# Kernel optimization log

Hardware: AMD Instinct MI355X
Metric: run time of the kernel (lower is better)

The kernel has to match this reference:

```python
import jax, jax.numpy as jnp
import numpy as np

X_SIZE, NUM_NEURONS, Z_SIZE = 2048, 4096, 64
D = X_SIZE + NUM_NEURONS + Z_SIZE  # 6208
TOPK, ZTOPK = 16, 8
EPS_TIE = 1e-9
RND = 0.5  # stand-in for random.random(); tie indicator t is 0 w.p. 1 for continuous inputs


def setup_inputs() -> dict:
    key = jax.random.key(0)
    k1, k2, k3, k4, k5 = jax.random.split(key, 5)
    x = jax.random.normal(k1, (X_SIZE,), dtype=jnp.float32)
    z = jax.random.normal(k2, (Z_SIZE,), dtype=jnp.float32)
    y_response = jax.random.uniform(k3, (NUM_NEURONS,), dtype=jnp.float32)
    neurons = jax.random.normal(k4, (D, D), dtype=jnp.float32)
    ages = 1.0 + 9.0 * jax.random.uniform(k5, (D,), dtype=jnp.float32)  # ages >= 1
    return {"x": x, "z": z, "y_response": y_response, "neurons": neurons, "ages": ages}


def _update_rows(neurons, ages, inpt, idx, vals):
    # Faithful to update_neuron_weights, including the (1,k)@(k,D) row-mix
    # that broadcasts the same mixed row to all k winner rows.
    a = ages[idx]                                   # (k,)
    upd = (vals / a)[:, None] * inpt[None, :]       # (k, D)
    mix = jnp.einsum('k,kd->d', (a - 1.0) / a, neurons[idx])  # (D,)
    new_rows = mix[None, :] + upd                   # (k, D)
    norm = jnp.sqrt(jnp.sum(new_rows * new_rows, axis=1, keepdims=True)) + 1e-12
    neurons = neurons.at[idx].set(new_rows / norm)
    ages = ages.at[idx].add(1.0)
    return neurons, ages


def reference(x, z, y_response, neurons, ages):
    # Steady-state path: num_neurons_init == max_num_neurons (> topk),
    # supervized_z = supervized_x = None, xtopk = None.
    x0, x1 = 0, X_SIZE
    y0, y1 = X_SIZE, X_SIZE + NUM_NEURONS
    z0 = X_SIZE + NUM_NEURONS

    inpt = jnp.concatenate([x, y_response, z])      # (D,)
    response = neurons @ inpt                       # (D,)
    final = jnp.zeros_like(response)

    # --- z path: top-(ztopk) winners, normalized against runner-up ---
    zvals, zidx = jax.lax.top_k(response[z0:], ZTOPK + 1)
    gz = z0 + zidx
    final = final.at[gz[:-1]].set((zvals[:-1] - zvals[-1]) / (zvals[0] - zvals[-1]))
    neurons, ages = _update_rows(neurons, ages, inpt, gz[:-1], zvals[:-1])

    # --- x path (xtopk None, unsupervised): normalize full x response ---
    rx = response[x0:x1]
    tx = jnp.where(jnp.all(rx == 0.0), 1.0, 0.0)
    xvals = rx / (jnp.max(rx) + EPS_TIE * tx * RND)
    final = final.at[x0:x1].set(xvals)
    xidx = jnp.arange(x0, x1)
    neurons, ages = _update_rows(neurons, ages, inpt, xidx[:-1], xvals[:-1])

    # --- y path: fully grown net -> topk winner-take-most branch ---
    yvals, yidx = jax.lax.top_k(response[y0:y1], TOPK + 1)
    gy = y0 + yidx
    ty = jnp.where(jnp.any(yvals[:-1] == yvals[-1]), 1.0, 0.0)
    final = final.at[gy[:-1]].set(
        (yvals[:-1] - yvals[-1]) / (yvals[0] - yvals[-1] + EPS_TIE * ty * RND))
    neurons, ages = _update_rows(neurons, ages, inpt, gy[:-1], yvals[:-1])

    z_response = final[z0:]
    return z_response, final, neurons, ages
```

## Files before the change

kernel.cpp:

```cpp
#include <hip/hip_runtime.h>
#include <math.h>

typedef float v4f __attribute__((ext_vector_type(4)));

#define XS 2048
#define NN 4096
#define ZS 64
#define DD 6208
#define D4 1552
#define Z0 (XS + NN)
#define TOPK 16
#define ZTOPK 8
#define EPS_TIE 1e-9f
#define RNDC 0.5f
#define NXUPD 2047

#define OUT_FINAL 64
#define OUT_NEUR  (64 + DD)
#define OUT_AGES  (OUT_NEUR + (size_t)DD * DD)

#define WS_RESP   0
#define WS_INPT   DD
#define WS_MIXX   (2 * DD)
#define WS_MIXZ   (3 * DD)
#define WS_MIXY   (4 * DD)
#define WS_SCAL   (5 * DD)
#define WS_SELROW (WS_SCAL + 32)
#define WS_SELC   (WS_SELROW + 24)
#define WS_SELW   (WS_SELC + 24)
#define WS_TOTAL  (WS_SELW + 32)

#define XBLKS 1024
#define CSPL  388

__device__ __forceinline__ v4f ld4(const float* p) { return *(const v4f*)p; }
__device__ __forceinline__ v4f v4z() { v4f v; v.x = v.y = v.z = v.w = 0.f; return v; }
__device__ __forceinline__ float dot4(v4f a, v4f b) {
  return fmaf(a.x, b.x, fmaf(a.y, b.y, fmaf(a.z, b.z, a.w * b.w)));
}
__device__ __forceinline__ v4f load_inpt(const float* x, const float* yr,
                                         const float* zv, int c) {
  int col = c * 4;
  if (col < XS) return ld4(x + col);
  if (col < Z0) return ld4(yr + (col - XS));
  return ld4(zv + (col - Z0));
}

__global__ __launch_bounds__(256) void k_phase1(
    const float* __restrict__ x, const float* __restrict__ yr,
    const float* __restrict__ zv, const float* __restrict__ neurons,
    const float* __restrict__ ages, float* __restrict__ ws,
    float* __restrict__ outn)
{
  const int t = threadIdx.x;
  const int b = blockIdx.x;

  if (b < XBLKS) {
    const int rg = b >> 2, cs = b & 3;
    const int row0 = rg * 8;
    const int cbase = cs * CSPL;
    const int c0 = cbase + t;
    const int c1 = cbase + 256 + t;
    const bool has1 = (t < CSPL - 256);

    v4f i0 = load_inpt(x, yr, zv, c0);
    v4f i1 = has1 ? load_inpt(x, yr, zv, c1) : v4z();
    if (b < 4) {
      ((v4f*)(ws + WS_INPT))[c0] = i0;
      if (has1) ((v4f*)(ws + WS_INPT))[c1] = i1;
    }

    float wr[8];
    #pragma unroll
    for (int r = 0; r < 8; ++r) {
      float a = ages[row0 + r];
      wr[r] = (row0 + r < NXUPD) ? (a - 1.f) / a : 0.f;
    }

    float dot[8];
    v4f m0 = v4z(), m1 = v4z();
    #pragma unroll
    for (int r = 0; r < 8; ++r) {
      const int row = row0 + r;
      const float* rp = neurons + (size_t)row * DD;
      v4f a0 = ld4(rp + 4 * c0);
      v4f a1 = has1 ? ld4(rp + 4 * c1) : v4z();
      dot[r] = dot4(a0, i0) + dot4(a1, i1);
      m0 += wr[r] * a0;
      m1 += wr[r] * a1;
      if (row >= NXUPD) {
        __builtin_nontemporal_store(a0, (v4f*)(outn + (size_t)row * DD + 4 * c0));
        if (has1)
          __builtin_nontemporal_store(a1, (v4f*)(outn + (size_t)row * DD + 4 * c1));
      }
    }

    __shared__ float wred[4][8];
    const int lane = t & 63, wv = t >> 6;
    #pragma unroll
    for (int r = 0; r < 8; ++r) {
      float v = dot[r];
      #pragma unroll
      for (int m = 32; m >= 1; m >>= 1) v += __shfl_xor(v, m);
      if (lane == 0) wred[wv][r] = v;
    }
    __syncthreads();
    if (t < 8)
      atomicAdd(ws + WS_RESP + row0 + t,
                wred[0][t] + wred[1][t] + wred[2][t] + wred[3][t]);

    atomicAdd(ws + WS_MIXX + 4 * c0 + 0, m0.x);
    atomicAdd(ws + WS_MIXX + 4 * c0 + 1, m0.y);
    atomicAdd(ws + WS_MIXX + 4 * c0 + 2, m0.z);
    atomicAdd(ws + WS_MIXX + 4 * c0 + 3, m0.w);
    if (has1) {
      atomicAdd(ws + WS_MIXX + 4 * c1 + 0, m1.x);
      atomicAdd(ws + WS_MIXX + 4 * c1 + 1, m1.y);
      atomicAdd(ws + WS_MIXX + 4 * c1 + 2, m1.z);
      atomicAdd(ws + WS_MIXX + 4 * c1 + 3, m1.w);
    }
  } else {
    const int row = 2048 + (b - XBLKS);
    const float* rp = neurons + (size_t)row * DD;
    float* op = outn + (size_t)row * DD;
    float dot = 0.f;
    #pragma unroll
    for (int k = 0; k < 6; ++k) {
      const int c = t + 256 * k;
      v4f a = ld4(rp + 4 * c);
      v4f iv = load_inpt(x, yr, zv, c);
      dot += dot4(a, iv);
      __builtin_nontemporal_store(a, (v4f*)(op + 4 * c));
    }
    if (t < 16) {
      const int c = 1536 + t;
      v4f a = ld4(rp + 4 * c);
      v4f iv = ld4(zv + (4 * c - Z0));
      dot += dot4(a, iv);
      __builtin_nontemporal_store(a, (v4f*)(op + 4 * c));
    }
    __shared__ float red[4];
    const int lane = t & 63, wv = t >> 6;
    #pragma unroll
    for (int m = 32; m >= 1; m >>= 1) dot += __shfl_xor(dot, m);
    if (lane == 0) red[wv] = dot;
    __syncthreads();
    if (t == 0) ws[WS_RESP + row] = red[0] + red[1] + red[2] + red[3];
  }
}

__global__ __launch_bounds__(1024) void k_phase2(
    const float* __restrict__ ages, float* __restrict__ ws, float* __restrict__ out)
{
  const int t = threadIdx.x;
  __shared__ float sv[NN];
  __shared__ float swv[64];
  __shared__ int   swi[16];
  __shared__ float s_zval[ZTOPK + 1];
  __shared__ int   s_zidx[ZTOPK + 1];
  __shared__ float s_yval[TOPK + 1];
  __shared__ int   s_yidx[TOPK + 1];
  __shared__ float s_denx, s_ty;
  __shared__ float s_z64[ZS];

  float* resp = ws + WS_RESP;

  if (t < ZS) s_z64[t] = resp[Z0 + t];
  __syncthreads();
  if (t < 64) {
    float v = s_z64[t];
    for (int j = 0; j <= ZTOPK; ++j) {
      float bv = v; int bi = t;
      #pragma unroll
      for (int m = 1; m < 64; m <<= 1) {
        float ov = __shfl_xor(bv, m);
        int   oi = __shfl_xor(bi, m);
        if (ov > bv || (ov == bv && oi < bi)) { bv = ov; bi = oi; }
      }
      if (t == 0) { s_zval[j] = bv; s_zidx[j] = bi; }
      if (t == bi) v = -INFINITY;
    }
  }

  float lm = -INFINITY; int nz = 0;
  for (int i = t; i < XS; i += 1024) { float v = resp[i]; lm = fmaxf(lm, v); nz |= (v != 0.f); }
  #pragma unroll
  for (int m = 1; m < 64; m <<= 1) { lm = fmaxf(lm, __shfl_xor(lm, m)); nz |= __shfl_xor(nz, m); }
  if ((t & 63) == 0) { swv[t >> 6] = lm; swi[t >> 6] = nz; }
  __syncthreads();
  if (t == 0) {
    float m2 = -INFINITY; int n2 = 0;
    for (int q = 0; q < 16; ++q) { m2 = fmaxf(m2, swv[q]); n2 |= swi[q]; }
    float tx = n2 ? 0.f : 1.f;
    s_denx = m2 + EPS_TIE * tx * RNDC;
  }
  __syncthreads();

  for (int i = t; i < NN; i += 1024) sv[i] = resp[XS + i];
  __syncthreads();
  for (int j = 0; j <= TOPK; ++j) {
    float bv = -INFINITY; int bi = 0x7fffffff;
    for (int i = t; i < NN; i += 1024) { float v = sv[i]; if (v > bv || (v == bv && i < bi)) { bv = v; bi = i; } }
    #pragma unroll
    for (int m = 1; m < 64; m <<= 1) {
      float ov = __shfl_xor(bv, m); int oi = __shfl_xor(bi, m);
      if (ov > bv || (ov == bv && oi < bi)) { bv = ov; bi = oi; }
    }
    if ((t & 63) == 0) { swv[t >> 6] = bv; swi[t >> 6] = bi; }
    __syncthreads();
    if (t == 0) {
      float b2 = -INFINITY; int i2 = 0x7fffffff;
      for (int q = 0; q < 16; ++q)
        if (swv[q] > b2 || (swv[q] == b2 && swi[q] < i2)) { b2 = swv[q]; i2 = swi[q]; }
      s_yval[j] = b2; s_yidx[j] = i2; sv[i2] = -INFINITY;
    }
    __syncthreads();
  }
  if (t == 0) {
    float ty = 0.f;
    for (int q = 0; q < TOPK; ++q) if (s_yval[q] == s_yval[TOPK]) ty = 1.f;
    s_ty = ty;
  }
  __syncthreads();

  const float denx  = s_denx;
  const float zlast = s_zval[ZTOPK];
  const float zden  = s_zval[0] - zlast;
  const float ylast = s_yval[TOPK];
  const float yden  = s_yval[0] - ylast + EPS_TIE * s_ty * RNDC;
  float* fin = out + OUT_FINAL;
  for (int i = t; i < DD; i += 1024) {
    float v = 0.f;
    if (i < XS) v = resp[i] / denx;
    fin[i] = v;
  }
  __syncthreads();
  if (t < ZTOPK)                  fin[Z0 + s_zidx[t]] = (s_zval[t] - zlast) / zden;
  else if (t >= 32 && t < 32 + TOPK) { int k = t - 32; fin[XS + s_yidx[k]] = (s_yval[k] - ylast) / yden; }
  if (t >= 128 && t < 192) {
    int i = t - 128;
    float v = 0.f;
    for (int k = 0; k < ZTOPK; ++k) if (s_zidx[k] == i) v = (s_zval[k] - zlast) / zden;
    out[i] = v;
  }

  float* oag = out + OUT_AGES;
  for (int i = t; i < DD; i += 1024) oag[i] = ages[i] + ((i < NXUPD) ? 1.f : 0.f);
  __syncthreads();
  if (t < ZTOPK + TOPK) {
    int row = (t < ZTOPK) ? (Z0 + s_zidx[t]) : (XS + s_yidx[t - ZTOPK]);
    oag[row] = ages[row] + 1.f;
  }

  float sii = 0.f, smm = 0.f, smi = 0.f;
  float* inpt = ws + WS_INPT;
  float* mixx = ws + WS_MIXX;
  for (int i = t; i < DD; i += 1024) {
    float ip = inpt[i], mx = mixx[i];
    sii = fmaf(ip, ip, sii); smm = fmaf(mx, mx, smm); smi = fmaf(mx, ip, smi);
  }
  #pragma unroll
  for (int m = 1; m < 64; m <<= 1) {
    sii += __shfl_xor(sii, m); smm += __shfl_xor(smm, m); smi += __shfl_xor(smi, m);
  }
  __syncthreads();
  if ((t & 63) == 0) { int w = t >> 6; swv[w] = sii; swv[16 + w] = smm; swv[32 + w] = smi; }
  __syncthreads();
  if (t == 0) {
    float a = 0.f, b = 0.f, c = 0.f;
    for (int q = 0; q < 16; ++q) { a += swv[q]; b += swv[16 + q]; c += swv[32 + q]; }
    float* scal = ws + WS_SCAL;
    scal[0] = a; scal[1] = b; scal[2] = c; scal[7] = denx;
  }

  if (t < ZTOPK) {
    int row = Z0 + s_zidx[t];
    ((int*)(ws + WS_SELROW))[t] = row;
    float a = ages[row];
    ws[WS_SELC + t] = s_zval[t] / a;
    ws[WS_SELW + t] = (a - 1.f) / a;
  } else if (t >= 32 && t < 32 + TOPK) {
    int k = t - 32;
    int row = XS + s_yidx[k];
    ((int*)(ws + WS_SELROW))[ZTOPK + k] = row;
    float a = ages[row];
    ws[WS_SELC + ZTOPK + k] = s_yval[k] / a;
    ws[WS_SELW + ZTOPK + k] = (a - 1.f) / a;
  }
}

__global__ __launch_bounds__(256) void k_phase3a(
    const float* __restrict__ neurons, float* __restrict__ ws)
{
  const int b = blockIdx.x;
  const int t = threadIdx.x;
  const int row = ((const int*)(ws + WS_SELROW))[b];
  const float w = ws[WS_SELW + b];
  float* dst = ws + ((b < ZTOPK) ? WS_MIXZ : WS_MIXY);
  const float* src = neurons + (size_t)row * DD;
  #pragma unroll
  for (int k = 0; k < 6; ++k) {
    const int c = t + 256 * k;
    v4f a = ld4(src + 4 * c);
    atomicAdd(dst + 4 * c + 0, w * a.x);
    atomicAdd(dst + 4 * c + 1, w * a.y);
    atomicAdd(dst + 4 * c + 2, w * a.z);
    atomicAdd(dst + 4 * c + 3, w * a.w);
  }
  if (t < 16) {
    const int c = 1536 + t;
    v4f a = ld4(src + 4 * c);
    atomicAdd(dst + 4 * c + 0, w * a.x);
    atomicAdd(dst + 4 * c + 1, w * a.y);
    atomicAdd(dst + 4 * c + 2, w * a.z);
    atomicAdd(dst + 4 * c + 3, w * a.w);
  }
}

__global__ __launch_bounds__(1024) void k_phase3b(float* __restrict__ ws)
{
  const int t = threadIdx.x;
  __shared__ float red[64];
  float* inpt = ws + WS_INPT;
  float smmz = 0.f, smiz = 0.f, smmy = 0.f, smiy = 0.f;
  for (int i = t; i < DD; i += 1024) {
    float ip = inpt[i];
    float mz = ws[WS_MIXZ + i], my = ws[WS_MIXY + i];
    smmz = fmaf(mz, mz, smmz); smiz = fmaf(mz, ip, smiz);
    smmy = fmaf(my, my, smmy); smiy = fmaf(my, ip, smiy);
  }
  #pragma unroll
  for (int m = 1; m < 64; m <<= 1) {
    smmz += __shfl_xor(smmz, m); smiz += __shfl_xor(smiz, m);
    smmy += __shfl_xor(smmy, m); smiy += __shfl_xor(smiy, m);
  }
  __syncthreads();
  if ((t & 63) == 0) { int w = t >> 6; red[w] = smmz; red[16 + w] = smiz; red[32 + w] = smmy; red[48 + w] = smiy; }
  __syncthreads();
  if (t == 0) {
    float a = 0.f, b = 0.f, c = 0.f, d = 0.f;
    for (int q = 0; q < 16; ++q) { a += red[q]; b += red[16 + q]; c += red[32 + q]; d += red[48 + q]; }
    ws[WS_SCAL + 3] = a; ws[WS_SCAL + 4] = b; ws[WS_SCAL + 5] = c; ws[WS_SCAL + 6] = d;
  }
}

__global__ __launch_bounds__(256) void k_phase4(
    const float* __restrict__ ages, const float* __restrict__ ws,
    float* __restrict__ outn)
{
  const int b = blockIdx.x;
  const int t = threadIdx.x;
  const float sii = ws[WS_SCAL + 0];
  int row; float c, smm, smi; const float* mix;
  if (b < NXUPD) {
    row = b;
    float a = ages[row];
    c = (ws[WS_RESP + row] / ws[WS_SCAL + 7]) / a;
    mix = ws + WS_MIXX; smm = ws[WS_SCAL + 1]; smi = ws[WS_SCAL + 2];
  } else {
    int k = b - NXUPD;
    row = ((const int*)(ws + WS_SELROW))[k];
    c = ws[WS_SELC + k];
    if (k < ZTOPK) { mix = ws + WS_MIXZ; smm = ws[WS_SCAL + 3]; smi = ws[WS_SCAL + 4]; }
    else           { mix = ws + WS_MIXY; smm = ws[WS_SCAL + 5]; smi = ws[WS_SCAL + 6]; }
  }
  const float inv = 1.f / (sqrtf(fmaf(c, fmaf(c, sii, 2.f * smi), smm)) + 1e-12f);
  const float* inpt = ws + WS_INPT;
  float* dst = outn + (size_t)row * DD;
  #pragma unroll
  for (int k = 0; k < 6; ++k) {
    const int i = t + 256 * k;
    v4f m4 = ((const v4f*)(mix))[i];
    v4f i4 = ((const v4f*)(inpt))[i];
    v4f o = (m4 + c * i4) * inv;
    __builtin_nontemporal_store(o, (v4f*)dst + i);
  }
  if (t < 16) {
    const int i = 1536 + t;
    v4f m4 = ((const v4f*)(mix))[i];
    v4f i4 = ((const v4f*)(inpt))[i];
    v4f o = (m4 + c * i4) * inv;
    __builtin_nontemporal_store(o, (v4f*)dst + i);
  }
}

extern "C" void kernel_launch(void* const* d_in, const int* in_sizes, int n_in,
                              void* d_out, int out_size, void* d_ws, size_t ws_size,
                              hipStream_t stream)
{
  (void)in_sizes; (void)n_in; (void)out_size; (void)ws_size;
  const float* x    = (const float*)d_in[0];
  const float* zin  = (const float*)d_in[1];
  const float* yr   = (const float*)d_in[2];
  const float* neur = (const float*)d_in[3];
  const float* ages = (const float*)d_in[4];
  float* out = (float*)d_out;
  float* ws  = (float*)d_ws;

  hipMemsetAsync(d_ws, 0, (size_t)WS_TOTAL * sizeof(float), stream);
  k_phase1<<<XBLKS + (DD - XS), 256, 0, stream>>>(x, yr, zin, neur, ages, ws, out + OUT_NEUR);
  k_phase2<<<1, 1024, 0, stream>>>(ages, ws, out);
  k_phase3a<<<ZTOPK + TOPK, 256, 0, stream>>>(neur, ws);
  k_phase3b<<<1, 1024, 0, stream>>>(ws);
  k_phase4<<<NXUPD + ZTOPK + TOPK, 256, 0, stream>>>(ages, ws, out + OUT_NEUR);
}
```

Before: 359.2 us.

## Replace MIXX atomics with staged partials, parallelize top-k, offload ages/final init

Phase1 x-blocks now write their per-row-group mix partials into the output neuron buffer as scratch rows instead of issuing float atomics to a shared workspace vector. Extra blocks in phase3a then reduce those 256 partial rows column-wise. Phase2's single-block top-k is restructured into per-wave local top-k followed by a one-wave merge, which removes many block-wide barriers. Ages and zero-fill of final are moved into auxiliary phase1 blocks, and all norm reductions are merged into phase3b. The scratch use of the output buffer relies on phase4 later overwriting those rows, and it adds a strided column read over 256 rows.

```diff
diff --git a/kernel.cpp b/kernel.cpp
--- a/kernel.cpp
+++ b/kernel.cpp
@@ -32,6 +32,10 @@
 
 #define XBLKS 1024
 #define CSPL  388
+#define YZBLKS (DD - XS)
+#define AUXBLKS 11
+
+#define RBLKS 388
 
 __device__ __forceinline__ v4f ld4(const float* p) { return *(const v4f*)p; }
 __device__ __forceinline__ v4f v4z() { v4f v; v.x = v.y = v.z = v.w = 0.f; return v; }
@@ -45,15 +49,24 @@
   if (col < Z0) return ld4(yr + (col - XS));
   return ld4(zv + (col - Z0));
 }
+__device__ __forceinline__ v4f wred4(v4f a) {
+  #pragma unroll
+  for (int m = 32; m >= 1; m >>= 1) {
+    a.x += __shfl_xor(a.x, m); a.y += __shfl_xor(a.y, m);
+    a.z += __shfl_xor(a.z, m); a.w += __shfl_xor(a.w, m);
+  }
+  return a;
+}
 
 __global__ __launch_bounds__(256) void k_phase1(
     const float* __restrict__ x, const float* __restrict__ yr,
     const float* __restrict__ zv, const float* __restrict__ neurons,
     const float* __restrict__ ages, float* __restrict__ ws,
-    float* __restrict__ outn)
+    float* __restrict__ out)
 {
   const int t = threadIdx.x;
   const int b = blockIdx.x;
+  float* outn = out + OUT_NEUR;
 
   if (b < XBLKS) {
     const int rg = b >> 2, cs = b & 3;
@@ -109,17 +122,10 @@
       atomicAdd(ws + WS_RESP + row0 + t,
                 wred[0][t] + wred[1][t] + wred[2][t] + wred[3][t]);
 
-    atomicAdd(ws + WS_MIXX + 4 * c0 + 0, m0.x);
-    atomicAdd(ws + WS_MIXX + 4 * c0 + 1, m0.y);
-    atomicAdd(ws + WS_MIXX + 4 * c0 + 2, m0.z);
-    atomicAdd(ws + WS_MIXX + 4 * c0 + 3, m0.w);
-    if (has1) {
-      atomicAdd(ws + WS_MIXX + 4 * c1 + 0, m1.x);
-      atomicAdd(ws + WS_MIXX + 4 * c1 + 1, m1.y);
-      atomicAdd(ws + WS_MIXX + 4 * c1 + 2, m1.z);
-      atomicAdd(ws + WS_MIXX + 4 * c1 + 3, m1.w);
-    }
-  } else {
+    float* pm = outn + (size_t)rg * DD;
+    *(v4f*)(pm + 4 * c0) = m0;
+    if (has1) *(v4f*)(pm + 4 * c1) = m1;
+  } else if (b < XBLKS + YZBLKS) {
     const int row = 2048 + (b - XBLKS);
     const float* rp = neurons + (size_t)row * DD;
     float* op = outn + (size_t)row * DD;
@@ -146,6 +152,19 @@
     if (lane == 0) red[wv] = dot;
     __syncthreads();
     if (t == 0) ws[WS_RESP + row] = red[0] + red[1] + red[2] + red[3];
+  } else {
+    const int e = b - (XBLKS + YZBLKS);
+    const int base = e * 1024;
+    #pragma unroll
+    for (int k = 0; k < 4; ++k) {
+      int j = base + t + 256 * k;
+      if (j < DD) {
+        out[OUT_AGES + j] = ages[j] + ((j < NXUPD) ? 1.f : 0.f);
+      } else {
+        int f = j - DD;
+        if (f < DD - XS) out[OUT_FINAL + XS + f] = 0.f;
+      }
+    }
   }
 }
 
@@ -153,194 +172,217 @@
     const float* __restrict__ ages, float* __restrict__ ws, float* __restrict__ out)
 {
   const int t = threadIdx.x;
-  __shared__ float sv[NN];
-  __shared__ float swv[64];
-  __shared__ int   swi[16];
+  const int lane = t & 63, wv = t >> 6;
+  __shared__ float s_candv[16 * (TOPK + 1)];
+  __shared__ int   s_candi[16 * (TOPK + 1)];
   __shared__ float s_zval[ZTOPK + 1];
   __shared__ int   s_zidx[ZTOPK + 1];
   __shared__ float s_yval[TOPK + 1];
   __shared__ int   s_yidx[TOPK + 1];
+  __shared__ float s_red[16];
+  __shared__ int   s_redi[16];
   __shared__ float s_denx, s_ty;
-  __shared__ float s_z64[ZS];
 
   float* resp = ws + WS_RESP;
-
-  if (t < ZS) s_z64[t] = resp[Z0 + t];
-  __syncthreads();
-  if (t < 64) {
-    float v = s_z64[t];
-    for (int j = 0; j <= ZTOPK; ++j) {
-      float bv = v; int bi = t;
+  float* fin  = out + OUT_FINAL;
+  float* oag  = out + OUT_AGES;
+
+  {
+    float v0 = resp[t], v1 = resp[t + 1024];
+    float lm = fmaxf(v0, v1);
+    int nz = (v0 != 0.f) | (v1 != 0.f);
+    #pragma unroll
+    for (int m = 1; m < 64; m <<= 1) { lm = fmaxf(lm, __shfl_xor(lm, m)); nz |= __shfl_xor(nz, m); }
+    if (lane == 0) { s_red[wv] = lm; s_redi[wv] = nz; }
+  }
+
+  {
+    float v[4]; int id[4];
+    #pragma unroll
+    for (int q = 0; q < 4; ++q) { int i = (wv << 8) + (q << 6) + lane; id[q] = i; v[q] = resp[XS + i]; }
+    for (int j = 0; j <= TOPK; ++j) {
+      float bv = v[0]; int bi = id[0];
+      #pragma unroll
+      for (int q = 1; q < 4; ++q)
+        if (v[q] > bv || (v[q] == bv && id[q] < bi)) { bv = v[q]; bi = id[q]; }
       #pragma unroll
       for (int m = 1; m < 64; m <<= 1) {
-        float ov = __shfl_xor(bv, m);
-        int   oi = __shfl_xor(bi, m);
+        float ov = __shfl_xor(bv, m); int oi = __shfl_xor(bi, m);
         if (ov > bv || (ov == bv && oi < bi)) { bv = ov; bi = oi; }
       }
-      if (t == 0) { s_zval[j] = bv; s_zidx[j] = bi; }
-      if (t == bi) v = -INFINITY;
-    }
-  }
-
-  float lm = -INFINITY; int nz = 0;
-  for (int i = t; i < XS; i += 1024) { float v = resp[i]; lm = fmaxf(lm, v); nz |= (v != 0.f); }
-  #pragma unroll
-  for (int m = 1; m < 64; m <<= 1) { lm = fmaxf(lm, __shfl_xor(lm, m)); nz |= __shfl_xor(nz, m); }
-  if ((t & 63) == 0) { swv[t >> 6] = lm; swi[t >> 6] = nz; }
+      if (lane == 0) { s_candv[wv * (TOPK + 1) + j] = bv; s_candi[wv * (TOPK + 1) + j] = bi; }
+      #pragma unroll
+      for (int q = 0; q < 4; ++q) if (id[q] == bi) v[q] = -INFINITY;
+    }
+  }
+
+  if (wv == 0) {
+    float v = resp[Z0 + lane];
+    for (int j = 0; j <= ZTOPK; ++j) {
+      float bv = v; int bi = lane;
+      #pragma unroll
+      for (int m = 1; m < 64; m <<= 1) {
+        float ov = __shfl_xor(bv, m); int oi = __shfl_xor(bi, m);
+        if (ov > bv || (ov == bv && oi < bi)) { bv = ov; bi = oi; }
+      }
+      if (lane == 0) { s_zval[j] = bv; s_zidx[j] = bi; }
+      if (lane == bi) v = -INFINITY;
+    }
+  }
+
   __syncthreads();
-  if (t == 0) {
+
+  if (t == 64) {
     float m2 = -INFINITY; int n2 = 0;
-    for (int q = 0; q < 16; ++q) { m2 = fmaxf(m2, swv[q]); n2 |= swi[q]; }
-    float tx = n2 ? 0.f : 1.f;
-    s_denx = m2 + EPS_TIE * tx * RNDC;
+    for (int q = 0; q < 16; ++q) { m2 = fmaxf(m2, s_red[q]); n2 |= s_redi[q]; }
+    float dx = m2 + EPS_TIE * (n2 ? 0.f : 1.f) * RNDC;
+    s_denx = dx;
+    ws[WS_SCAL + 7] = dx;
+  }
+  if (wv == 0) {
+    float mv[5]; int mi[5];
+    #pragma unroll
+    for (int q = 0; q < 5; ++q) {
+      int k = lane + (q << 6);
+      if (k < 16 * (TOPK + 1)) { mv[q] = s_candv[k]; mi[q] = s_candi[k]; }
+      else { mv[q] = -INFINITY; mi[q] = 0x7fffffff; }
+    }
+    for (int j = 0; j <= TOPK; ++j) {
+      float bv = mv[0]; int bi = mi[0];
+      #pragma unroll
+      for (int q = 1; q < 5; ++q)
+        if (mv[q] > bv || (mv[q] == bv && mi[q] < bi)) { bv = mv[q]; bi = mi[q]; }
+      #pragma unroll
+      for (int m = 1; m < 64; m <<= 1) {
+        float ov = __shfl_xor(bv, m); int oi = __shfl_xor(bi, m);
+        if (ov > bv || (ov == bv && oi < bi)) { bv = ov; bi = oi; }
+      }
+      if (lane == 0) { s_yval[j] = bv; s_yidx[j] = bi; }
+      #pragma unroll
+      for (int q = 0; q < 5; ++q) if (mi[q] == bi) mv[q] = -INFINITY;
+    }
+    if (lane == 0) {
+      float ty = 0.f;
+      for (int q = 0; q < TOPK; ++q) if (s_yval[q] == s_yval[TOPK]) ty = 1.f;
+      s_ty = ty;
+    }
   }
   __syncthreads();
 
-  for (int i = t; i < NN; i += 1024) sv[i] = resp[XS + i];
-  __syncthreads();
-  for (int j = 0; j <= TOPK; ++j) {
-    float bv = -INFINITY; int bi = 0x7fffffff;
-    for (int i = t; i < NN; i += 1024) { float v = sv[i]; if (v > bv || (v == bv && i < bi)) { bv = v; bi = i; } }
-    #pragma unroll
-    for (int m = 1; m < 64; m <<= 1) {
-      float ov = __shfl_xor(bv, m); int oi = __shfl_xor(bi, m);
-      if (ov > bv || (ov == bv && oi < bi)) { bv = ov; bi = oi; }
-    }
-    if ((t & 63) == 0) { swv[t >> 6] = bv; swi[t >> 6] = bi; }
-    __syncthreads();
-    if (t == 0) {
-      float b2 = -INFINITY; int i2 = 0x7fffffff;
-      for (int q = 0; q < 16; ++q)
-        if (swv[q] > b2 || (swv[q] == b2 && swi[q] < i2)) { b2 = swv[q]; i2 = swi[q]; }
-      s_yval[j] = b2; s_yidx[j] = i2; sv[i2] = -INFINITY;
-    }
-    __syncthreads();
-  }
-  if (t == 0) {
-    float ty = 0.f;
-    for (int q = 0; q < TOPK; ++q) if (s_yval[q] == s_yval[TOPK]) ty = 1.f;
-    s_ty = ty;
-  }
-  __syncthreads();
-
   const float denx  = s_denx;
+  fin[t]        = resp[t] / denx;
+  fin[t + 1024] = resp[t + 1024] / denx;
+
   const float zlast = s_zval[ZTOPK];
   const float zden  = s_zval[0] - zlast;
   const float ylast = s_yval[TOPK];
   const float yden  = s_yval[0] - ylast + EPS_TIE * s_ty * RNDC;
-  float* fin = out + OUT_FINAL;
-  for (int i = t; i < DD; i += 1024) {
-    float v = 0.f;
-    if (i < XS) v = resp[i] / denx;
-    fin[i] = v;
-  }
-  __syncthreads();
-  if (t < ZTOPK)                  fin[Z0 + s_zidx[t]] = (s_zval[t] - zlast) / zden;
-  else if (t >= 32 && t < 32 + TOPK) { int k = t - 32; fin[XS + s_yidx[k]] = (s_yval[k] - ylast) / yden; }
-  if (t >= 128 && t < 192) {
+
+  if (t < ZTOPK) {
+    int zi = s_zidx[t];
+    int row = Z0 + zi;
+    fin[row] = (s_zval[t] - zlast) / zden;
+    float a = ages[row];
+    ((int*)(ws + WS_SELROW))[t] = row;
+    ws[WS_SELC + t] = s_zval[t] / a;
+    ws[WS_SELW + t] = (a - 1.f) / a;
+    oag[row] = a + 1.f;
+  } else if (t >= 32 && t < 32 + TOPK) {
+    int k = t - 32;
+    int row = XS + s_yidx[k];
+    fin[row] = (s_yval[k] - ylast) / yden;
+    float a = ages[row];
+    ((int*)(ws + WS_SELROW))[ZTOPK + k] = row;
+    ws[WS_SELC + ZTOPK + k] = s_yval[k] / a;
+    ws[WS_SELW + ZTOPK + k] = (a - 1.f) / a;
+    oag[row] = a + 1.f;
+  } else if (t >= 128 && t < 192) {
     int i = t - 128;
     float v = 0.f;
     for (int k = 0; k < ZTOPK; ++k) if (s_zidx[k] == i) v = (s_zval[k] - zlast) / zden;
     out[i] = v;
   }
-
-  float* oag = out + OUT_AGES;
-  for (int i = t; i < DD; i += 1024) oag[i] = ages[i] + ((i < NXUPD) ? 1.f : 0.f);
-  __syncthreads();
-  if (t < ZTOPK + TOPK) {
-    int row = (t < ZTOPK) ? (Z0 + s_zidx[t]) : (XS + s_yidx[t - ZTOPK]);
-    oag[row] = ages[row] + 1.f;
-  }
-
-  float sii = 0.f, smm = 0.f, smi = 0.f;
-  float* inpt = ws + WS_INPT;
-  float* mixx = ws + WS_MIXX;
+}
+
+__global__ __launch_bounds__(256) void k_phase3a(
+    const float* __restrict__ neurons, const float* __restrict__ outn,
+    float* __restrict__ ws)
+{
+  const int b = blockIdx.x;
+  const int t = threadIdx.x;
+  if (b < ZTOPK + TOPK) {
+    const int row = ((const int*)(ws + WS_SELROW))[b];
+    const float w = ws[WS_SELW + b];
+    float* dst = ws + ((b < ZTOPK) ? WS_MIXZ : WS_MIXY);
+    const float* src = neurons + (size_t)row * DD;
+    #pragma unroll
+    for (int k = 0; k < 6; ++k) {
+      const int c = t + 256 * k;
+      v4f a = ld4(src + 4 * c);
+      atomicAdd(dst + 4 * c + 0, w * a.x);
+      atomicAdd(dst + 4 * c + 1, w * a.y);
+      atomicAdd(dst + 4 * c + 2, w * a.z);
+      atomicAdd(dst + 4 * c + 3, w * a.w);
+    }
+    if (t < 16) {
+      const int c = 1536 + t;
+      v4f a = ld4(src + 4 * c);
+      atomicAdd(dst + 4 * c + 0, w * a.x);
+      atomicAdd(dst + 4 * c + 1, w * a.y);
+      atomicAdd(dst + 4 * c + 2, w * a.z);
+      atomicAdd(dst + 4 * c + 3, w * a.w);
+    }
+  } else {
+    const int g = b - (ZTOPK + TOPK);
+    const int cb = 4 * g;
+    const float* pr = outn + (size_t)t * DD + 4 * cb;
+    v4f a0 = ld4(pr), a1 = ld4(pr + 4), a2 = ld4(pr + 8), a3 = ld4(pr + 12);
+    a0 = wred4(a0); a1 = wred4(a1); a2 = wred4(a2); a3 = wred4(a3);
+    __shared__ v4f sred[4][4];
+    if ((t & 63) == 0) {
+      int w = t >> 6;
+      sred[w][0] = a0; sred[w][1] = a1; sred[w][2] = a2; sred[w][3] = a3;
+    }
+    __syncthreads();
+    if (t < 4) {
+      v4f s = sred[0][t] + sred[1][t] + sred[2][t] + sred[3][t];
+      *(v4f*)(ws + WS_MIXX + 4 * (cb + t)) = s;
+    }
+  }
+}
+
+__global__ __launch_bounds__(1024) void k_phase3b(float* __restrict__ ws)
+{
+  const int t = threadIdx.x;
+  __shared__ float red[16][7];
+  const float* inpt = ws + WS_INPT;
+  float s0 = 0.f, s1 = 0.f, s2 = 0.f, s3 = 0.f, s4 = 0.f, s5 = 0.f, s6 = 0.f;
   for (int i = t; i < DD; i += 1024) {
-    float ip = inpt[i], mx = mixx[i];
-    sii = fmaf(ip, ip, sii); smm = fmaf(mx, mx, smm); smi = fmaf(mx, ip, smi);
+    float ip = inpt[i];
+    float mx = ws[WS_MIXX + i], mz = ws[WS_MIXZ + i], my = ws[WS_MIXY + i];
+    s0 = fmaf(ip, ip, s0);
+    s1 = fmaf(mx, mx, s1); s2 = fmaf(mx, ip, s2);
+    s3 = fmaf(mz, mz, s3); s4 = fmaf(mz, ip, s4);
+    s5 = fmaf(my, my, s5); s6 = fmaf(my, ip, s6);
   }
   #pragma unroll
   for (int m = 1; m < 64; m <<= 1) {
-    sii += __shfl_xor(sii, m); smm += __shfl_xor(smm, m); smi += __shfl_xor(smi, m);
-  }
-  __syncthreads();
-  if ((t & 63) == 0) { int w = t >> 6; swv[w] = sii; swv[16 + w] = smm; swv[32 + w] = smi; }
+    s0 += __shfl_xor(s0, m); s1 += __shfl_xor(s1, m); s2 += __shfl_xor(s2, m);
+    s3 += __shfl_xor(s3, m); s4 += __shfl_xor(s4, m); s5 += __shfl_xor(s5, m);
+    s6 += __shfl_xor(s6, m);
+  }
+  if ((t & 63) == 0) {
+    int w = t >> 6;
+    red[w][0] = s0; red[w][1] = s1; red[w][2] = s2; red[w][3] = s3;
+    red[w][4] = s4; red[w][5] = s5; red[w][6] = s6;
+  }
   __syncthreads();
   if (t == 0) {
-    float a = 0.f, b = 0.f, c = 0.f;
-    for (int q = 0; q < 16; ++q) { a += swv[q]; b += swv[16 + q]; c += swv[32 + q]; }
+    float a[7] = {0.f, 0.f, 0.f, 0.f, 0.f, 0.f, 0.f};
+    for (int q = 0; q < 16; ++q)
+      for (int k = 0; k < 7; ++k) a[k] += red[q][k];
     float* scal = ws + WS_SCAL;
-    scal[0] = a; scal[1] = b; scal[2] = c; scal[7] = denx;
-  }
-
-  if (t < ZTOPK) {
-    int row = Z0 + s_zidx[t];
-    ((int*)(ws + WS_SELROW))[t] = row;
-    float a = ages[row];
-    ws[WS_SELC + t] = s_zval[t] / a;
-    ws[WS_SELW + t] = (a - 1.f) / a;
-  } else if (t >= 32 && t < 32 + TOPK) {
-    int k = t - 32;
-    int row = XS + s_yidx[k];
-    ((int*)(ws + WS_SELROW))[ZTOPK + k] = row;
-    float a = ages[row];
-    ws[WS_SELC + ZTOPK + k] = s_yval[k] / a;
-    ws[WS_SELW + ZTOPK + k] = (a - 1.f) / a;
-  }
-}
-
-__global__ __launch_bounds__(256) void k_phase3a(
-    const float* __restrict__ neurons, float* __restrict__ ws)
-{
-  const int b = blockIdx.x;
-  const int t = threadIdx.x;
-  const int row = ((const int*)(ws + WS_SELROW))[b];
-  const float w = ws[WS_SELW + b];
-  float* dst = ws + ((b < ZTOPK) ? WS_MIXZ : WS_MIXY);
-  const float* src = neurons + (size_t)row * DD;
-  #pragma unroll
-  for (int k = 0; k < 6; ++k) {
-    const int c = t + 256 * k;
-    v4f a = ld4(src + 4 * c);
-    atomicAdd(dst + 4 * c + 0, w * a.x);
-    atomicAdd(dst + 4 * c + 1, w * a.y);
-    atomicAdd(dst + 4 * c + 2, w * a.z);
-    atomicAdd(dst + 4 * c + 3, w * a.w);
-  }
-  if (t < 16) {
-    const int c = 1536 + t;
-    v4f a = ld4(src + 4 * c);
-    atomicAdd(dst + 4 * c + 0, w * a.x);
-    atomicAdd(dst + 4 * c + 1, w * a.y);
-    atomicAdd(dst + 4 * c + 2, w * a.z);
-    atomicAdd(dst + 4 * c + 3, w * a.w);
-  }
-}
-
-__global__ __launch_bounds__(1024) void k_phase3b(float* __restrict__ ws)
-{
-  const int t = threadIdx.x;
-  __shared__ float red[64];
-  float* inpt = ws + WS_INPT;
-  float smmz = 0.f, smiz = 0.f, smmy = 0.f, smiy = 0.f;
-  for (int i = t; i < DD; i += 1024) {
-    float ip = inpt[i];
-    float mz = ws[WS_MIXZ + i], my = ws[WS_MIXY + i];
-    smmz = fmaf(mz, mz, smmz); smiz = fmaf(mz, ip, smiz);
-    smmy = fmaf(my, my, smmy); smiy = fmaf(my, ip, smiy);
-  }
-  #pragma unroll
-  for (int m = 1; m < 64; m <<= 1) {
-    smmz += __shfl_xor(smmz, m); smiz += __shfl_xor(smiz, m);
-    smmy += __shfl_xor(smmy, m); smiy += __shfl_xor(smiy, m);
-  }
-  __syncthreads();
-  if ((t & 63) == 0) { int w = t >> 6; red[w] = smmz; red[16 + w] = smiz; red[32 + w] = smmy; red[48 + w] = smiy; }
-  __syncthreads();
-  if (t == 0) {
-    float a = 0.f, b = 0.f, c = 0.f, d = 0.f;
-    for (int q = 0; q < 16; ++q) { a += red[q]; b += red[16 + q]; c += red[32 + q]; d += red[48 + q]; }
-    ws[WS_SCAL + 3] = a; ws[WS_SCAL + 4] = b; ws[WS_SCAL + 5] = c; ws[WS_SCAL + 6] = d;
+    for (int k = 0; k < 7; ++k) scal[k] = a[k];
   }
 }
 
@@ -398,9 +440,9 @@
   float* ws  = (float*)d_ws;
 
   hipMemsetAsync(d_ws, 0, (size_t)WS_TOTAL * sizeof(float), stream);
-  k_phase1<<<XBLKS + (DD - XS), 256, 0, stream>>>(x, yr, zin, neur, ages, ws, out + OUT_NEUR);
+  k_phase1<<<XBLKS + YZBLKS + AUXBLKS, 256, 0, stream>>>(x, yr, zin, neur, ages, ws, out);
   k_phase2<<<1, 1024, 0, stream>>>(ages, ws, out);
-  k_phase3a<<<ZTOPK + TOPK, 256, 0, stream>>>(neur, ws);
+  k_phase3a<<<ZTOPK + TOPK + RBLKS, 256, 0, stream>>>(neur, out + OUT_NEUR, ws);
   k_phase3b<<<1, 1024, 0, stream>>>(ws);
   k_phase4<<<NXUPD + ZTOPK + TOPK, 256, 0, stream>>>(ages, ws, out + OUT_NEUR);
 }
```

Measured after the change: 321.0 us. 10.6% less time.
